# Optimization experiments

Hardware: AMD Instinct MI355X
Metric: run time of the kernel (lower is better)

## Reference

```python
import jax, jax.numpy as jnp
import numpy as np

THRESHOLD = 0.9
EPS = 1e-12  # F.normalize eps


def setup_inputs() -> dict:
    key = jax.random.key(0)
    clusters = jax.random.normal(key, (64, 256, 768), dtype=jnp.float32)
    return {"clusters": clusters}


def _collapse(clusters, threshold):
    B, Q, D = clusters.shape
    # F.normalize(clusters, dim=-1): divide by L2 norm clamped to eps
    norm = jnp.maximum(jnp.linalg.norm(clusters, axis=-1, keepdims=True), EPS)
    nc = clusters / norm
    sim = jnp.einsum('bqd,bkd->bqk', nc, nc)              # [B, Q, Q]
    # torch loop condition: collapse_mask[:, i, j].any() -> any over batch
    pair_flag = jnp.any(sim > threshold, axis=0)          # [Q, Q] bool, fixed before merging

    # loop order: i outer, j inner (j > i) == row-major upper triangle
    ii, jj = jnp.triu_indices(Q, k=1)
    flags = pair_flag[ii, jj]                              # [Q*(Q-1)/2]

    def step(c, x):
        i, j, f = x
        ci = jnp.take(c, i, axis=1)                        # [B, D]
        cj = jnp.take(c, j, axis=1)
        new_i = jnp.where(f, (ci + cj) * 0.5, ci)
        c = c.at[:, i].set(new_i)
        c = c.at[:, j].set(jnp.where(f, new_i, cj))        # clusters[:, j] = clusters[:, i]
        return c, None

    out, _ = jax.lax.scan(step, clusters, (ii, jj, flags))
    return out


def reference(clusters):
    return _collapse(clusters, THRESHOLD)
```

## Files before the change

kernel.cpp:

```cpp
#include <hip/hip_runtime.h>
#include <math.h>

#define BB 64
#define QQ 256
#define DD 768
#define THR 0.9f
#define EPSN 1e-12f

#define OFF_FBITS  0
#define OFF_COUNT  8192
#define OFF_PAIRS  8320
#define OFF_M      138880

using f32x4 = __attribute__((ext_vector_type(4))) float;
using s16x8 = __attribute__((ext_vector_type(8))) short;

struct Frag { float4 lo, hi; };

#define GL2LDS(g, l) __builtin_amdgcn_global_load_lds( \
    (const __attribute__((address_space(1))) void*)(g), \
    (__attribute__((address_space(3))) void*)(l), 16, 0, 0)

#define SCHED_FENCE() __builtin_amdgcn_sched_barrier(0)

__device__ __forceinline__ s16x8 cvt(const Frag& f) {
    union { s16x8 s; unsigned u[4]; } r;
    r.u[0] = __builtin_amdgcn_perm(__float_as_uint(f.lo.y), __float_as_uint(f.lo.x), 0x07060302u);
    r.u[1] = __builtin_amdgcn_perm(__float_as_uint(f.lo.w), __float_as_uint(f.lo.z), 0x07060302u);
    r.u[2] = __builtin_amdgcn_perm(__float_as_uint(f.hi.y), __float_as_uint(f.hi.x), 0x07060302u);
    r.u[3] = __builtin_amdgcn_perm(__float_as_uint(f.hi.w), __float_as_uint(f.hi.z), 0x07060302u);
    return r.s;
}
__device__ __forceinline__ float sq8(const Frag& f) {
    return f.lo.x*f.lo.x + f.lo.y*f.lo.y + f.lo.z*f.lo.z + f.lo.w*f.lo.w
         + f.hi.x*f.hi.x + f.hi.y*f.hi.y + f.hi.z*f.hi.z + f.hi.w*f.hi.w;
}

__global__ __launch_bounds__(256) void zero_kernel(unsigned* __restrict__ fbits,
                                                   int* __restrict__ count,
                                                   int* __restrict__ nflag) {
    int t = threadIdx.x;
    #pragma unroll
    for (int k = 0; k < 8; ++k) fbits[t + k * 256] = 0u;
    if (t == 0) { *count = 0; *nflag = 0; }
}

__global__ __launch_bounds__(256) void flags_kernel(const float* __restrict__ in,
                                                    float* __restrict__ out,
                                                    unsigned* __restrict__ fbits,
                                                    int* __restrict__ nflag) {
    __shared__ float lds[12288];

    int orig = blockIdx.x;
    int g = (orig & 7) * 80 + (orig >> 3);
    int tp = g % 10, b = g / 10;
    int it = 0, rem = tp, rowlen = 4;
    while (rem >= rowlen) { rem -= rowlen; ++it; --rowlen; }
    int jt = it + rem;
    int i0 = it * 64, j0 = jt * 64;

    int w = threadIdx.x >> 6, lane = threadIdx.x & 63;
    int wr = w >> 1, wc = w & 1;
    int r  = lane & 15, kg = lane >> 4;

    const float* base = in + (size_t)b * QQ * DD;

    int lr = lane >> 3;
    int lq = lane & 7;
    int swz = (lq ^ lr) * 4;
    const float* pA0 = base + (size_t)(i0 + w * 16 + lr) * DD + swz;
    const float* pA1 = pA0 + (size_t)8 * DD;
    const float* pB0 = base + (size_t)(j0 + w * 16 + lr) * DD + swz;
    const float* pB1 = pB0 + (size_t)8 * DD;

    f32x4 acc[2][2] = {};
    float4 ns = {0.f, 0.f, 0.f, 0.f};

    const f32x4* in4 = (const f32x4*)in;
    f32x4* out4 = (f32x4*)out;
    f32x4 cr[3];
    auto CLD = [&](int s) {
        int off = tp * 24 + s; off = off < 192 ? off : 191;
        cr[s % 3] = in4[(size_t)b * 49152 + (size_t)off * 256 + threadIdx.x];
    };
    auto CST = [&](int s) {
        int off = tp * 24 + s; off = off < 192 ? off : 191;
        __builtin_nontemporal_store(cr[s % 3],
            &out4[(size_t)b * 49152 + (size_t)off * 256 + threadIdx.x]);
    };

    auto STAGE = [&](int buf, int c) {
        int k0 = c * 32;
        float* L = lds + buf * 4096 + w * 512;
        GL2LDS(pA0 + k0, L);
        GL2LDS(pA1 + k0, L + 256);
        GL2LDS(pB0 + k0, L + 2048);
        GL2LDS(pB1 + k0, L + 2048 + 256);
    };
    auto RD = [&](const float* L, int row) {
        int qlo = (2 * kg) ^ (row & 7);
        Frag f;
        f.lo = *(const float4*)&L[row * 32 + qlo * 4];
        f.hi = *(const float4*)&L[row * 32 + (qlo ^ 1) * 4];
        return f;
    };
    auto CHUNK = [&](int buf) {
        const float* LA = lds + buf * 4096;
        const float* LB = LA + 2048;
        Frag fa0 = RD(LA, wr * 32 + r);
        Frag fa1 = RD(LA, wr * 32 + r + 16);
        Frag fb0 = RD(LB, wc * 32 + r);
        Frag fb1 = RD(LB, wc * 32 + r + 16);
        ns.x += sq8(fa0); ns.y += sq8(fa1); ns.z += sq8(fb0); ns.w += sq8(fb1);
        s16x8 a0 = cvt(fa0), a1 = cvt(fa1), b0 = cvt(fb0), b1 = cvt(fb1);
        acc[0][0] = __builtin_amdgcn_mfma_f32_16x16x32_bf16(a0, b0, acc[0][0], 0, 0, 0);
        acc[0][1] = __builtin_amdgcn_mfma_f32_16x16x32_bf16(a0, b1, acc[0][1], 0, 0, 0);
        acc[1][0] = __builtin_amdgcn_mfma_f32_16x16x32_bf16(a1, b0, acc[1][0], 0, 0, 0);
        acc[1][1] = __builtin_amdgcn_mfma_f32_16x16x32_bf16(a1, b1, acc[1][1], 0, 0, 0);
    };

    CLD(0); STAGE(0, 0);
    SCHED_FENCE();
    CLD(1); STAGE(1, 1);
    #pragma unroll
    for (int c = 0; c < 24; ++c) {
        SCHED_FENCE();
        if (c < 22) { CLD(c + 2); STAGE((c + 2) % 3, c + 2); }
        SCHED_FENCE();
        if (c == 0)       asm volatile("s_waitcnt vmcnt(10)");
        else if (c == 1)  asm volatile("s_waitcnt vmcnt(11)");
        else if (c <= 21) asm volatile("s_waitcnt vmcnt(12)");
        else if (c == 22) asm volatile("s_waitcnt vmcnt(7)");
        else              asm volatile("s_waitcnt vmcnt(2)");
        SCHED_FENCE();
        __builtin_amdgcn_s_barrier();
        CHUNK(c % 3);
        CST(c);
        SCHED_FENCE();
        __builtin_amdgcn_s_barrier();
    }

    ns.x += __shfl_xor(ns.x, 16); ns.x += __shfl_xor(ns.x, 32);
    ns.y += __shfl_xor(ns.y, 16); ns.y += __shfl_xor(ns.y, 32);
    ns.z += __shfl_xor(ns.z, 16); ns.z += __shfl_xor(ns.z, 32);
    ns.w += __shfl_xor(ns.w, 16); ns.w += __shfl_xor(ns.w, 32);

    float njc0 = fmaxf(sqrtf(ns.z), EPSN);
    float njc1 = fmaxf(sqrtf(ns.w), EPSN);

    bool any = false;
    #pragma unroll
    for (int m = 0; m < 2; ++m) {
        float nsa = (m == 0) ? ns.x : ns.y;
        #pragma unroll
        for (int rr = 0; rr < 4; ++rr) {
            float ni2 = __shfl(nsa, kg * 4 + rr);
            float ni  = fmaxf(sqrtf(ni2), EPSN);
            int i = i0 + wr * 32 + m * 16 + kg * 4 + rr;
            int j = j0 + wc * 32 + r;
            if (j > i && acc[m][0][rr] > THR * ni * njc0) {
                int idx = i * QQ + j;
                atomicOr(&fbits[idx >> 5], 1u << (idx & 31)); any = true;
            }
            j += 16;
            if (j > i && acc[m][1][rr] > THR * ni * njc1) {
                int idx = i * QQ + j;
                atomicOr(&fbits[idx >> 5], 1u << (idx & 31)); any = true;
            }
        }
    }
    if (any) atomicAdd(nflag, 1);
}

__global__ __launch_bounds__(256) void compact_merge_kernel(const unsigned* __restrict__ fbits,
                                                            int* __restrict__ pairs,
                                                            int* __restrict__ count,
                                                            const int* __restrict__ nflag,
                                                            float* __restrict__ M) {
    int t = threadIdx.x;
    if (*nflag == 0) { if (t == 0) *count = 0; return; }

    const int P  = QQ * (QQ - 1) / 2;
    const int CH = (P + 255) / 256;
    int L0 = t * CH;
    int L1 = min(L0 + CH, P);

    int i = 0, cum = 0;
    while (i < QQ - 1 && cum + (QQ - 1 - i) <= L0) { cum += (QQ - 1 - i); ++i; }
    int j = i + 1 + (L0 - cum);

    auto getbit = [&](int ii, int jj) -> int {
        int idx = ii * QQ + jj;
        return (fbits[idx >> 5] >> (idx & 31)) & 1;
    };

    int cnt = 0;
    { int ii = i, jj = j;
      for (int L = L0; L < L1; ++L) {
          cnt += getbit(ii, jj);
          if (++jj == QQ) { ++ii; jj = ii + 1; }
      } }

    __shared__ int sc[256];
    sc[t] = cnt;
    __syncthreads();
    for (int off = 1; off < 256; off <<= 1) {
        int u = (t >= off) ? sc[t - off] : 0;
        __syncthreads();
        sc[t] += u;
        __syncthreads();
    }
    int bse = sc[t] - cnt;
    if (t == 255) *count = sc[255];

    { int ii = i, jj = j;
      for (int L = L0; L < L1; ++L) {
          if (getbit(ii, jj)) pairs[bse++] = (ii << 16) | jj;
          if (++jj == QQ) { ++ii; jj = ii + 1; }
      } }
    __syncthreads();

    int n = sc[255];
    for (int rr = 0; rr < QQ; ++rr) M[rr * QQ + t] = (rr == t) ? 1.f : 0.f;
    for (int s = 0; s < n; ++s) {
        int pr = pairs[s];
        int pi = pr >> 16, pj = pr & 0xffff;
        float nv = 0.5f * (M[pi * QQ + t] + M[pj * QQ + t]);
        M[pi * QQ + t] = nv;
        M[pj * QQ + t] = nv;
    }
}

__global__ __launch_bounds__(256) void applyM_kernel(const float* __restrict__ in,
                                                     const float* __restrict__ M,
                                                     float* __restrict__ out,
                                                     const int* __restrict__ count) {
    if (*count == 0) return;
    int b = blockIdx.x, qt = blockIdx.y;
    int t = threadIdx.x;
    for (int q = qt * 64; q < qt * 64 + 64; ++q) {
        float a0 = 0.f, a1 = 0.f, a2 = 0.f;
        for (int k = 0; k < QQ; ++k) {
            float m = M[q * QQ + k];
            if (m == 0.f) continue;
            const float* src = in + ((size_t)b * QQ + k) * DD;
            a0 += m * src[t];
            a1 += m * src[t + 256];
            a2 += m * src[t + 512];
        }
        float* dst = out + ((size_t)b * QQ + q) * DD;
        dst[t] = a0; dst[t + 256] = a1; dst[t + 512] = a2;
    }
}

extern "C" void kernel_launch(void* const* d_in, const int* in_sizes, int n_in,
                              void* d_out, int out_size, void* d_ws, size_t ws_size,
                              hipStream_t stream) {
    const float* in = (const float*)d_in[0];
    float* out = (float*)d_out;
    char* ws = (char*)d_ws;

    unsigned* fbits = (unsigned*)(ws + OFF_FBITS);
    int*   count = (int*)  (ws + OFF_COUNT);
    int*   nflag = (int*)  (ws + OFF_COUNT + 4);
    int*   pairs = (int*)  (ws + OFF_PAIRS);
    float* M     = (float*)(ws + OFF_M);

    zero_kernel<<<dim3(1), dim3(256), 0, stream>>>(fbits, count, nflag);
    flags_kernel<<<dim3(640), dim3(256), 0, stream>>>(in, out, fbits, nflag);
    compact_merge_kernel<<<dim3(1), dim3(256), 0, stream>>>(fbits, pairs, count, nflag, M);
    applyM_kernel<<<dim3(BB, 4), dim3(256), 0, stream>>>(in, M, out, count);
}
```

Baseline: 38.00 us.

## Pre-convert inputs to bf16 fragment layout before the Gram flag kernel

Adds a conversion kernel that turns the fp32 clusters into bf16 stored directly in MFMA fragment order and accumulates per-row squared norms with atomics. A new gram kernel then loads fragments straight from global memory, with no LDS staging, and applies the threshold against the product of the norms instead of normalizing inside the loop. The aim is to cut LDS traffic and fp32 reload cost in the similarity pass. In exchange it adds an extra kernel launch, a 24 MB workspace write and read, and float atomics for the norms. The old path is kept as a fallback when the workspace is too small.

```diff
diff --git a/kernel.cpp b/kernel.cpp
--- a/kernel.cpp
+++ b/kernel.cpp
@@ -11,6 +11,10 @@
 #define OFF_COUNT  8192
 #define OFF_PAIRS  8320
 #define OFF_M      138880
+#define OFF_NSQ    401024
+#define OFF_X      466944
+#define X_BYTES    25165824
+#define WS_NEED    ((size_t)OFF_X + X_BYTES)
 
 using f32x4 = __attribute__((ext_vector_type(4))) float;
 using s16x8 = __attribute__((ext_vector_type(8))) short;
@@ -38,19 +42,49 @@
 
 __global__ __launch_bounds__(256) void zero_kernel(unsigned* __restrict__ fbits,
                                                    int* __restrict__ count,
+                                                   int* __restrict__ nflag,
+                                                   float* __restrict__ nsq) {
+    int t = threadIdx.x;
+    #pragma unroll
+    for (int k = 0; k < 8; ++k) fbits[t + k * 256] = 0u;
+    #pragma unroll
+    for (int k = 0; k < 64; ++k) nsq[t + k * 256] = 0.f;
+    if (t == 0) { *count = 0; *nflag = 0; }
+}
+
+__global__ __launch_bounds__(256) void conv_kernel(const float* __restrict__ in,
+                                                   short* __restrict__ X,
+                                                   float* __restrict__ nsq) {
+    int beta = blockIdx.x;
+    int w = threadIdx.x >> 6, l = threadIdx.x & 63;
+    int b = beta >> 3, sub = beta & 7;
+    int rg = sub * 2 + (w >> 1);
+    int h  = w & 1;
+    int row = rg * 16 + (l & 15), kg = l >> 4;
+
+    const float* src = in + ((size_t)b * QQ + row) * DD + kg * 8;
+    short* dst = X + ((size_t)(b * 16 + rg) * 24) * 512 + (size_t)l * 8;
+
+    float s = 0.f;
+    #pragma unroll 6
+    for (int c = h * 12; c < h * 12 + 12; ++c) {
+        Frag f;
+        f.lo = *(const float4*)(src + c * 32);
+        f.hi = *(const float4*)(src + c * 32 + 4);
+        s += sq8(f);
+        *(s16x8*)(dst + (size_t)c * 512) = cvt(f);
+    }
+    s += __shfl_xor(s, 16);
+    s += __shfl_xor(s, 32);
+    if (l < 16) atomicAdd(&nsq[b * QQ + rg * 16 + l], s);
+}
+
+__global__ __launch_bounds__(256) void gram_kernel(const short* __restrict__ X,
+                                                   const float* __restrict__ nsq,
+                                                   const float* __restrict__ in,
+                                                   float* __restrict__ out,
+                                                   unsigned* __restrict__ fbits,
                                                    int* __restrict__ nflag) {
-    int t = threadIdx.x;
-    #pragma unroll
-    for (int k = 0; k < 8; ++k) fbits[t + k * 256] = 0u;
-    if (t == 0) { *count = 0; *nflag = 0; }
-}
-
-__global__ __launch_bounds__(256) void flags_kernel(const float* __restrict__ in,
-                                                    float* __restrict__ out,
-                                                    unsigned* __restrict__ fbits,
-                                                    int* __restrict__ nflag) {
-    __shared__ float lds[12288];
-
     int orig = blockIdx.x;
     int g = (orig & 7) * 80 + (orig >> 3);
     int tp = g % 10, b = g / 10;
@@ -59,14 +93,86 @@
     int jt = it + rem;
     int i0 = it * 64, j0 = jt * 64;
 
+    int tid = threadIdx.x;
+    int w = tid >> 6, l = tid & 63;
+    int wr = w >> 1, wc = w & 1;
+    int r = l & 15, kg = l >> 4;
+
+    const s16x8* base = (const s16x8*)X;
+    int rgA = it * 4 + wr * 2;
+    int rgB = jt * 4 + wc * 2;
+    const s16x8* pA0 = base + ((size_t)(b * 16 + rgA) * 24) * 64 + l;
+    const s16x8* pA1 = base + ((size_t)(b * 16 + rgA + 1) * 24) * 64 + l;
+    const s16x8* pB0 = base + ((size_t)(b * 16 + rgB) * 24) * 64 + l;
+    const s16x8* pB1 = base + ((size_t)(b * 16 + rgB + 1) * 24) * 64 + l;
+
+    const f32x4* in4 = (const f32x4*)in;
+    f32x4* out4 = (f32x4*)out;
+    f32x4 cr[3];
+    auto SLOT = [&](int s) -> size_t {
+        int idx = tp * 20 + s; idx = idx < 191 ? idx : 191;
+        return (size_t)b * 49152 + (size_t)idx * 256 + tid;
+    };
+
+    f32x4 acc[2][2] = {};
+    #pragma unroll 4
+    for (int c = 0; c < 24; ++c) {
+        if (c < 20) cr[c % 3] = in4[SLOT(c)];
+        s16x8 a0 = pA0[c * 64];
+        s16x8 a1 = pA1[c * 64];
+        s16x8 b0 = pB0[c * 64];
+        s16x8 b1 = pB1[c * 64];
+        acc[0][0] = __builtin_amdgcn_mfma_f32_16x16x32_bf16(a0, b0, acc[0][0], 0, 0, 0);
+        acc[0][1] = __builtin_amdgcn_mfma_f32_16x16x32_bf16(a0, b1, acc[0][1], 0, 0, 0);
+        acc[1][0] = __builtin_amdgcn_mfma_f32_16x16x32_bf16(a1, b0, acc[1][0], 0, 0, 0);
+        acc[1][1] = __builtin_amdgcn_mfma_f32_16x16x32_bf16(a1, b1, acc[1][1], 0, 0, 0);
+        if (c >= 2 && c - 2 < 20)
+            __builtin_nontemporal_store(cr[(c - 2) % 3], &out4[SLOT(c - 2)]);
+    }
+
+    const float* nb = nsq + b * QQ;
+    bool any = false;
+    #pragma unroll
+    for (int m = 0; m < 2; ++m) {
+        #pragma unroll
+        for (int rr = 0; rr < 4; ++rr) {
+            int i = i0 + wr * 32 + m * 16 + kg * 4 + rr;
+            float thr_i = THR * fmaxf(sqrtf(nb[i]), EPSN);
+            int j = j0 + wc * 32 + r;
+            if (j > i && acc[m][0][rr] > thr_i * fmaxf(sqrtf(nb[j]), EPSN)) {
+                int idx = i * QQ + j;
+                atomicOr(&fbits[idx >> 5], 1u << (idx & 31)); any = true;
+            }
+            j += 16;
+            if (j > i && acc[m][1][rr] > thr_i * fmaxf(sqrtf(nb[j]), EPSN)) {
+                int idx = i * QQ + j;
+                atomicOr(&fbits[idx >> 5], 1u << (idx & 31)); any = true;
+            }
+        }
+    }
+    if (any) atomicAdd(nflag, 1);
+}
+
+__global__ __launch_bounds__(256) void flags_kernel(const float* __restrict__ in,
+                                                    float* __restrict__ out,
+                                                    unsigned* __restrict__ fbits,
+                                                    int* __restrict__ nflag) {
+    __shared__ float lds[12288];
+
+    int orig = blockIdx.x;
+    int g = (orig & 7) * 80 + (orig >> 3);
+    int tp = g % 10, b = g / 10;
+    int it = 0, rem = tp, rowlen = 4;
+    while (rem >= rowlen) { rem -= rowlen; ++it; --rowlen; }
+    int jt = it + rem;
+    int i0 = it * 64, j0 = jt * 64;
+
     int w = threadIdx.x >> 6, lane = threadIdx.x & 63;
     int wr = w >> 1, wc = w & 1;
     int r  = lane & 15, kg = lane >> 4;
 
     const float* base = in + (size_t)b * QQ * DD;
-
-    int lr = lane >> 3;
-    int lq = lane & 7;
+    int lr = lane >> 3, lq = lane & 7;
     int swz = (lq ^ lr) * 4;
     const float* pA0 = base + (size_t)(i0 + w * 16 + lr) * DD + swz;
     const float* pA1 = pA0 + (size_t)8 * DD;
@@ -88,7 +194,6 @@
         __builtin_nontemporal_store(cr[s % 3],
             &out4[(size_t)b * 49152 + (size_t)off * 256 + threadIdx.x]);
     };
-
     auto STAGE = [&](int buf, int c) {
         int k0 = c * 32;
         float* L = lds + buf * 4096 + w * 512;
@@ -265,9 +370,16 @@
     int*   nflag = (int*)  (ws + OFF_COUNT + 4);
     int*   pairs = (int*)  (ws + OFF_PAIRS);
     float* M     = (float*)(ws + OFF_M);
-
-    zero_kernel<<<dim3(1), dim3(256), 0, stream>>>(fbits, count, nflag);
-    flags_kernel<<<dim3(640), dim3(256), 0, stream>>>(in, out, fbits, nflag);
+    float* nsq   = (float*)(ws + OFF_NSQ);
+    short* X     = (short*)(ws + OFF_X);
+
+    zero_kernel<<<dim3(1), dim3(256), 0, stream>>>(fbits, count, nflag, nsq);
+    if (ws_size >= WS_NEED) {
+        conv_kernel<<<dim3(512), dim3(256), 0, stream>>>(in, X, nsq);
+        gram_kernel<<<dim3(640), dim3(256), 0, stream>>>(X, nsq, in, out, fbits, nflag);
+    } else {
+        flags_kernel<<<dim3(640), dim3(256), 0, stream>>>(in, out, fbits, nflag);
+    }
     compact_merge_kernel<<<dim3(1), dim3(256), 0, stream>>>(fbits, pairs, count, nflag, M);
     applyM_kernel<<<dim3(BB, 4), dim3(256), 0, stream>>>(in, M, out, count);
 }
```

After: 53.77 us. 41.5% more time.
